# Performance work log

Measured on AMD Instinct MI355X. Metric: run time of the kernel, lower is better.

The kernel has to match this reference:

```python
import jax, jax.numpy as jnp
import numpy as np

NEG_INF = -1e9  # matches the TF additive-mask constant


def setup_inputs() -> dict:
    key = jax.random.key(0)
    k1, k2, k3 = jax.random.split(key, 3)
    B, Tq, Tk, D = 8, 2048, 2048, 1024
    decoder_outputs = jax.random.normal(k1, (B, Tq, D), dtype=jnp.float32)
    encoder_outputs = jax.random.normal(k2, (B, Tk, D), dtype=jnp.float32)
    encoder_mask = jax.random.randint(k3, (B, Tk), 0, 2, dtype=jnp.int32)
    return {
        "decoder_outputs": decoder_outputs,
        "encoder_outputs": encoder_outputs,
        "encoder_mask": encoder_mask,
    }


def reference(decoder_outputs, encoder_outputs, encoder_mask):
    # score[b, q, k] = <dec[b, q], enc[b, k]>  (no 1/sqrt(d) scaling in original)
    score = jnp.einsum("bqd,bkd->bqk", decoder_outputs, encoder_outputs)
    m = encoder_mask.astype(score.dtype)[:, None, :]  # [B, 1, Tk]
    score = score + (1.0 - m) * NEG_INF
    attention_weights = jax.nn.softmax(score, axis=-1)
    context_vector = jnp.einsum("bqk,bkd->bqd", attention_weights, encoder_outputs)
    return (context_vector, attention_weights)
```

## Files before the change

### kernel.cpp

```cpp
#include <hip/hip_runtime.h>
#include <cstddef>
#include <cstdint>

typedef _Float16 f16x8 __attribute__((ext_vector_type(8)));
typedef _Float16 f16x4 __attribute__((ext_vector_type(4)));
typedef float f32x4 __attribute__((ext_vector_type(4)));

static constexpr int BATCH = 8;
static constexpr int TQ = 2048;
static constexpr int TK = 2048;
static constexpr int DIM = 1024;
static constexpr size_t CTX_ELEMS = (size_t)BATCH * TQ * DIM;
static constexpr size_t ATT_ELEMS = (size_t)BATCH * TQ * TK;

static constexpr size_t WS_DEC = 0;
static constexpr size_t WS_ENC = WS_DEC + CTX_ELEMS;
static constexpr size_t WS_ENCT = WS_ENC + CTX_ELEMS;
static constexpr size_t WS_W = WS_ENCT + CTX_ELEMS;
static constexpr size_t WS_NEEDED_BYTES = (WS_W + ATT_ELEMS) * 2;

__device__ __forceinline__ void async16(const void* g, const void* l) {
  __builtin_amdgcn_global_load_lds(
      (const __attribute__((address_space(1))) unsigned int*)g,
      (__attribute__((address_space(3))) unsigned int*)l, 16, 0, 0);
}

__device__ __forceinline__ f16x8 cvt8(float4 a, float4 b) {
  f16x8 h;
  h[0] = (_Float16)a.x; h[1] = (_Float16)a.y; h[2] = (_Float16)a.z; h[3] = (_Float16)a.w;
  h[4] = (_Float16)b.x; h[5] = (_Float16)b.y; h[6] = (_Float16)b.z; h[7] = (_Float16)b.w;
  return h;
}


__global__ __launch_bounds__(256) void convert_dec_kernel(
    const float* __restrict__ dec, _Float16* __restrict__ dec16) {
  size_t i = ((size_t)blockIdx.x * 256 + threadIdx.x) * 8;
  float4 a = *(const float4*)(dec + i);
  float4 b = *(const float4*)(dec + i + 4);
  *(f16x8*)(dec16 + i) = cvt8(a, b);
}

__global__ __launch_bounds__(256) void convert_enc_kernel(
    const float* __restrict__ enc, _Float16* __restrict__ enc16,
    _Float16* __restrict__ encT) {
  __shared__ _Float16 sT[64 * 72];
  const int k0 = blockIdx.x * 64, d0 = blockIdx.y * 64, b = blockIdx.z;
  const int t = threadIdx.x;
  const int krow = t >> 2;
  const int dcol = (t & 3) * 16;

  const float* src = enc + ((size_t)b * TK + k0 + krow) * DIM + d0 + dcol;
  float4 f0 = *(const float4*)(src);
  float4 f1 = *(const float4*)(src + 4);
  float4 f2 = *(const float4*)(src + 8);
  float4 f3 = *(const float4*)(src + 12);
  _Float16 h[16];
#pragma unroll
  for (int i = 0; i < 4; i++) {
    h[i]      = (_Float16)((&f0.x)[i]);
    h[i + 4]  = (_Float16)((&f1.x)[i]);
    h[i + 8]  = (_Float16)((&f2.x)[i]);
    h[i + 12] = (_Float16)((&f3.x)[i]);
  }
  _Float16* dsts = enc16 + ((size_t)b * TK + k0 + krow) * DIM + d0 + dcol;
  *(f16x8*)dsts = *(const f16x8*)&h[0];
  *(f16x8*)(dsts + 8) = *(const f16x8*)&h[8];
#pragma unroll
  for (int i = 0; i < 16; i++)
    sT[(dcol + i) * 72 + krow] = h[i];
  __syncthreads();

  const int drow = t >> 2;
  const int kg = (t & 3) * 16;
  f16x8 v0 = *(const f16x8*)&sT[drow * 72 + kg];
  f16x8 v1 = *(const f16x8*)&sT[drow * 72 + kg + 8];
  _Float16* dst = encT + ((size_t)b * DIM + d0 + drow) * TK + k0 + kg;
  *(f16x8*)dst = v0;
  *(f16x8*)(dst + 8) = v1;
}

template <int M, int N, int K>
__global__ __launch_bounds__(256, 2) void gemm_nt(
    const _Float16* __restrict__ A, const _Float16* __restrict__ B,
    float* __restrict__ C) {
  __shared__ _Float16 sA[2][256 * 32];
  __shared__ _Float16 sB[2][128 * 32];

  const int b = blockIdx.x, nt = blockIdx.y, mt = blockIdx.z;
  const int t = threadIdx.x;
  const int lane = t & 63, w = t >> 6;
  const int tm = lane & 15, quad = lane >> 4;

  const _Float16* Ab = A + ((size_t)b * M + mt * 256) * K;
  const _Float16* Bb = B + ((size_t)b * N + nt * 128) * K;

  const int srow = lane >> 2;
  const int scol = (lane & 3) * 8;

  f32x4 acc[4][8] = {};

  for (int k0 = 0; k0 < K; k0 += 64) {
    __syncthreads();
#pragma unroll
    for (int s = 0; s < 2; s++) {
#pragma unroll
      for (int i = 0; i < 4; i++)
        async16(Ab + (size_t)(w * 64 + 16 * i + srow) * K + k0 + s * 32 + scol,
                &sA[s][(w * 64 + 16 * i) * 32]);
#pragma unroll
      for (int i = 0; i < 2; i++)
        async16(Bb + (size_t)(w * 32 + 16 * i + srow) * K + k0 + s * 32 + scol,
                &sB[s][(w * 32 + 16 * i) * 32]);
    }
    __syncthreads();

#pragma unroll
    for (int s = 0; s < 2; s++) {
      f16x8 aF[4], bF[8];
#pragma unroll
      for (int i = 0; i < 4; i++)
        aF[i] = *(const f16x8*)&sA[s][(w * 64 + i * 16 + tm) * 32 + quad * 8];
#pragma unroll
      for (int j = 0; j < 8; j++)
        bF[j] = *(const f16x8*)&sB[s][(j * 16 + tm) * 32 + quad * 8];

#pragma unroll
      for (int i = 0; i < 4; i++)
#pragma unroll
        for (int j = 0; j < 8; j++)
          acc[i][j] = __builtin_amdgcn_mfma_f32_16x16x32_f16(aF[i], bF[j], acc[i][j], 0, 0, 0);
    }
  }

#pragma unroll
  for (int i = 0; i < 4; i++) {
#pragma unroll
    for (int rr = 0; rr < 4; rr++) {
      size_t rowoff = ((size_t)b * M + mt * 256 + w * 64 + i * 16 + quad * 4 + rr) * (size_t)N;
#pragma unroll
      for (int j = 0; j < 8; j++)
        C[rowoff + nt * 128 + j * 16 + tm] = acc[i][j][rr];
    }
  }
}

__global__ __launch_bounds__(256) void softmax_kernel(
    float* __restrict__ S, const int* __restrict__ mask, _Float16* __restrict__ W16) {
  const int row = blockIdx.x;
  const int b = row >> 11;
  float* srow = S + (size_t)row * TK;
  const int* mrow = mask + (size_t)b * TK;
  const int t = threadIdx.x;

  float4 s0 = *(const float4*)(srow + t * 8);
  float4 s1 = *(const float4*)(srow + t * 8 + 4);
  int4 m0 = *(const int4*)(mrow + t * 8);
  int4 m1 = *(const int4*)(mrow + t * 8 + 4);

  float v[8] = {s0.x, s0.y, s0.z, s0.w, s1.x, s1.y, s1.z, s1.w};
  const int mm[8] = {m0.x, m0.y, m0.z, m0.w, m1.x, m1.y, m1.z, m1.w};
#pragma unroll
  for (int i = 0; i < 8; i++)
    if (!mm[i]) v[i] += -1e9f;

  float mx = v[0];
#pragma unroll
  for (int i = 1; i < 8; i++) mx = fmaxf(mx, v[i]);
#pragma unroll
  for (int off = 32; off > 0; off >>= 1) mx = fmaxf(mx, __shfl_down(mx, off));

  __shared__ float redm[4];
  __shared__ float reds[4];
  if ((t & 63) == 0) redm[t >> 6] = mx;
  __syncthreads();
  mx = fmaxf(fmaxf(redm[0], redm[1]), fmaxf(redm[2], redm[3]));

  float e[8];
  float lsum = 0.f;
#pragma unroll
  for (int i = 0; i < 8; i++) {
    e[i] = __expf(v[i] - mx);
    lsum += e[i];
  }
#pragma unroll
  for (int off = 32; off > 0; off >>= 1) lsum += __shfl_down(lsum, off);
  if ((t & 63) == 0) reds[t >> 6] = lsum;
  __syncthreads();
  const float inv = 1.0f / (reds[0] + reds[1] + reds[2] + reds[3]);

  float4 o0 = {e[0] * inv, e[1] * inv, e[2] * inv, e[3] * inv};
  float4 o1 = {e[4] * inv, e[5] * inv, e[6] * inv, e[7] * inv};
  *(float4*)(srow + t * 8) = o0;
  *(float4*)(srow + t * 8 + 4) = o1;
  if (W16) {
    f16x8 h;
    h[0] = (_Float16)o0.x; h[1] = (_Float16)o0.y; h[2] = (_Float16)o0.z; h[3] = (_Float16)o0.w;
    h[4] = (_Float16)o1.x; h[5] = (_Float16)o1.y; h[6] = (_Float16)o1.z; h[7] = (_Float16)o1.w;
    *(f16x8*)(W16 + (size_t)row * TK + t * 8) = h;
  }
}

static constexpr int BM = 128, BN = 128, BK = 32;
static constexpr int LDSS = 40;

__global__ __launch_bounds__(256) void score_kernel_fb(
    const float* __restrict__ dec, const float* __restrict__ enc,
    float* __restrict__ S) {
  __shared__ _Float16 sA[BM * LDSS];
  __shared__ _Float16 sB[BN * LDSS];
  const int nt = blockIdx.x, mt = blockIdx.y, b = blockIdx.z;
  const int t = threadIdx.x;
  const int lane = t & 63, wave = t >> 6;
  const int wm = wave >> 1, wn = wave & 1;
  const int tm = lane & 15, quad = lane >> 4;
  const float* Abase = dec + ((size_t)b * TQ + mt * BM) * DIM;
  const float* Bbase = enc + ((size_t)b * TK + nt * BN) * DIM;
  f32x4 acc[4][4] = {};
  const int r = t >> 2;
  const int c8 = (t & 3) * 8;
  for (int k0 = 0; k0 < DIM; k0 += BK) {
    float4 a0 = *(const float4*)(Abase + (size_t)r * DIM + k0 + c8);
    float4 a1 = *(const float4*)(Abase + (size_t)r * DIM + k0 + c8 + 4);
    float4 a2 = *(const float4*)(Abase + (size_t)(r + 64) * DIM + k0 + c8);
    float4 a3 = *(const float4*)(Abase + (size_t)(r + 64) * DIM + k0 + c8 + 4);
    float4 b0 = *(const float4*)(Bbase + (size_t)r * DIM + k0 + c8);
    float4 b1 = *(const float4*)(Bbase + (size_t)r * DIM + k0 + c8 + 4);
    float4 b2 = *(const float4*)(Bbase + (size_t)(r + 64) * DIM + k0 + c8);
    float4 b3 = *(const float4*)(Bbase + (size_t)(r + 64) * DIM + k0 + c8 + 4);
    __syncthreads();
    *(f16x8*)&sA[r * LDSS + c8] = cvt8(a0, a1);
    *(f16x8*)&sA[(r + 64) * LDSS + c8] = cvt8(a2, a3);
    *(f16x8*)&sB[r * LDSS + c8] = cvt8(b0, b1);
    *(f16x8*)&sB[(r + 64) * LDSS + c8] = cvt8(b2, b3);
    __syncthreads();
    f16x8 aF[4], bF[4];
#pragma unroll
    for (int i = 0; i < 4; i++)
      aF[i] = *(const f16x8*)&sA[(wm * 64 + i * 16 + tm) * LDSS + quad * 8];
#pragma unroll
    for (int j = 0; j < 4; j++)
      bF[j] = *(const f16x8*)&sB[(wn * 64 + j * 16 + tm) * LDSS + quad * 8];
#pragma unroll
    for (int i = 0; i < 4; i++)
#pragma unroll
      for (int j = 0; j < 4; j++)
        acc[i][j] = __builtin_amdgcn_mfma_f32_16x16x32_f16(aF[i], bF[j], acc[i][j], 0, 0, 0);
  }
#pragma unroll
  for (int i = 0; i < 4; i++) {
#pragma unroll
    for (int rr = 0; rr < 4; rr++) {
      size_t rowoff = ((size_t)b * TQ + mt * BM + wm * 64 + i * 16 + quad * 4 + rr) * (size_t)TK;
#pragma unroll
      for (int j = 0; j < 4; j++)
        S[rowoff + nt * BN + wn * 64 + j * 16 + tm] = acc[i][j][rr];
    }
  }
}

__global__ __launch_bounds__(256) void ctx_kernel_fb(
    const float* __restrict__ W, const float* __restrict__ enc,
    float* __restrict__ C) {
  __shared__ _Float16 sA[BM * LDSS];
  __shared__ _Float16 sB[BN * LDSS];
  const int nt = blockIdx.x;
  const int mt = blockIdx.y;
  const int b = blockIdx.z;
  const int t = threadIdx.x;
  const int lane = t & 63, wave = t >> 6;
  const int wm = wave >> 1, wn = wave & 1;
  const int tm = lane & 15, quad = lane >> 4;
  const float* Abase = W + ((size_t)b * TQ + mt * BM) * TK;
  const float* Ebase = enc + (size_t)b * TK * DIM + nt * BN;
  f32x4 acc[4][4] = {};
  const int r = t >> 2;
  const int c8 = (t & 3) * 8;
  const int kkB = (t & 7) * 4;
  const int nnB = (t >> 3) * 4;
  for (int k0 = 0; k0 < TK; k0 += BK) {
    float4 a0 = *(const float4*)(Abase + (size_t)r * TK + k0 + c8);
    float4 a1 = *(const float4*)(Abase + (size_t)r * TK + k0 + c8 + 4);
    float4 a2 = *(const float4*)(Abase + (size_t)(r + 64) * TK + k0 + c8);
    float4 a3 = *(const float4*)(Abase + (size_t)(r + 64) * TK + k0 + c8 + 4);
    float4 f[4];
#pragma unroll
    for (int i = 0; i < 4; i++)
      f[i] = *(const float4*)(Ebase + (size_t)(k0 + kkB + i) * DIM + nnB);
    __syncthreads();
    *(f16x8*)&sA[r * LDSS + c8] = cvt8(a0, a1);
    *(f16x8*)&sA[(r + 64) * LDSS + c8] = cvt8(a2, a3);
#pragma unroll
    for (int c = 0; c < 4; c++) {
      f16x4 h;
      h[0] = (_Float16)((&f[0].x)[c]);
      h[1] = (_Float16)((&f[1].x)[c]);
      h[2] = (_Float16)((&f[2].x)[c]);
      h[3] = (_Float16)((&f[3].x)[c]);
      *(f16x4*)&sB[(nnB + c) * LDSS + kkB] = h;
    }
    __syncthreads();
    f16x8 aF[4], bF[4];
#pragma unroll
    for (int i = 0; i < 4; i++)
      aF[i] = *(const f16x8*)&sA[(wm * 64 + i * 16 + tm) * LDSS + quad * 8];
#pragma unroll
    for (int j = 0; j < 4; j++)
      bF[j] = *(const f16x8*)&sB[(wn * 64 + j * 16 + tm) * LDSS + quad * 8];
#pragma unroll
    for (int i = 0; i < 4; i++)
#pragma unroll
      for (int j = 0; j < 4; j++)
        acc[i][j] = __builtin_amdgcn_mfma_f32_16x16x32_f16(aF[i], bF[j], acc[i][j], 0, 0, 0);
  }
#pragma unroll
  for (int i = 0; i < 4; i++) {
#pragma unroll
    for (int rr = 0; rr < 4; rr++) {
      size_t rowoff = ((size_t)b * TQ + mt * BM + wm * 64 + i * 16 + quad * 4 + rr) * (size_t)DIM;
#pragma unroll
      for (int j = 0; j < 4; j++)
        C[rowoff + nt * BN + wn * 64 + j * 16 + tm] = acc[i][j][rr];
    }
  }
}

extern "C" void kernel_launch(void* const* d_in, const int* in_sizes, int n_in,
                              void* d_out, int out_size, void* d_ws, size_t ws_size,
                              hipStream_t stream) {
  const float* dec = (const float*)d_in[0];
  const float* enc = (const float*)d_in[1];
  const int* mask = (const int*)d_in[2];

  float* ctx = (float*)d_out;
  float* attn = (float*)d_out + CTX_ELEMS;

  dim3 block(256);

  if (ws_size >= WS_NEEDED_BYTES) {
    _Float16* dec16 = (_Float16*)d_ws + WS_DEC;
    _Float16* enc16 = (_Float16*)d_ws + WS_ENC;
    _Float16* encT = (_Float16*)d_ws + WS_ENCT;
    _Float16* W16 = (_Float16*)d_ws + WS_W;

    convert_dec_kernel<<<dim3(CTX_ELEMS / (256 * 8)), block, 0, stream>>>(dec, dec16);
    convert_enc_kernel<<<dim3(TK / 64, DIM / 64, BATCH), block, 0, stream>>>(enc, enc16, encT);
    gemm_nt<TQ, TK, DIM><<<dim3(BATCH, TK / 128, TQ / 256), block, 0, stream>>>(dec16, enc16, attn);
    softmax_kernel<<<dim3(BATCH * TQ), block, 0, stream>>>(attn, mask, W16);
    gemm_nt<TQ, DIM, TK><<<dim3(BATCH, DIM / 128, TQ / 256), block, 0, stream>>>(W16, encT, ctx);
  } else {
    score_kernel_fb<<<dim3(TK / BN, TQ / BM, BATCH), block, 0, stream>>>(dec, enc, attn);
    softmax_kernel<<<dim3(BATCH * TQ), block, 0, stream>>>(attn, mask, nullptr);
    ctx_kernel_fb<<<dim3(DIM / BN, TQ / BM, BATCH), block, 0, stream>>>(attn, enc, ctx);
  }
}
```

Measured before the change: 502.7 us.

## Replace GEMM with 8-wave 256x256 tile kernel using software-pipelined LDS staging

Replaces the 256-thread 256x128-tile GEMM with a 512-thread, 8-wave kernel that computes 256x256 output tiles. Global-to-LDS async loads are split into half-K stages and issued two iterations ahead, with explicit vmcnt waits and barriers so loads overlap the MFMA work. It also raises MFMA issue priority around the compute blocks. The larger tile cuts global traffic per FLOP, but the 128 KB of LDS and the heavier register use may limit occupancy, and the hand-tuned waitcnt sequencing is fragile.

Measured after the change: 514.0 us. 2.2% more time.

```diff
diff --git a/kernel.cpp b/kernel.cpp
--- a/kernel.cpp
+++ b/kernel.cpp
@@ -80,67 +80,120 @@
   *(f16x8*)(dst + 8) = v1;
 }
 
+
+template <int KD>
+__device__ __forceinline__ void stage_half(const _Float16* __restrict__ Xb,
+                                           _Float16* slot, int khalf,
+                                           int w, int lane) {
+  const int kgl = w & 3;
+  const int rg0 = (w >> 2) * 2;
+  const _Float16* g = Xb + (size_t)(rg0 * 64 + lane) * KD + khalf + kgl * 8;
+  _Float16* l = slot + kgl * 2048 + rg0 * 512;
+  async16(g, l);
+  async16(g + (size_t)64 * KD, l + 512);
+}
+
+__device__ __forceinline__ void load4(f16x8 (&dst)[4], const _Float16* base) {
+#pragma unroll
+  for (int i = 0; i < 4; ++i) dst[i] = *(const f16x8*)(base + i * 128);
+}
+
+__device__ __forceinline__ void mfma16(f32x4 (&acc)[8][4], const f16x8 (&aF)[4],
+                                       const f16x8 (&bF)[4], int mh) {
+  __builtin_amdgcn_s_setprio(1);
+#pragma unroll
+  for (int i = 0; i < 4; ++i)
+#pragma unroll
+    for (int j = 0; j < 4; ++j)
+      acc[mh * 4 + i][j] = __builtin_amdgcn_mfma_f32_16x16x32_f16(
+          aF[i], bF[j], acc[mh * 4 + i][j], 0, 0, 0);
+  __builtin_amdgcn_s_setprio(0);
+}
+
 template <int M, int N, int K>
-__global__ __launch_bounds__(256, 2) void gemm_nt(
+__global__ __launch_bounds__(512, 2) void gemm8p(
     const _Float16* __restrict__ A, const _Float16* __restrict__ B,
     float* __restrict__ C) {
-  __shared__ _Float16 sA[2][256 * 32];
-  __shared__ _Float16 sB[2][128 * 32];
+  __shared__ _Float16 lds[65536];
+  constexpr int T = K / 64;
 
   const int b = blockIdx.x, nt = blockIdx.y, mt = blockIdx.z;
-  const int t = threadIdx.x;
-  const int lane = t & 63, w = t >> 6;
+  const int tid = threadIdx.x;
+  const int lane = tid & 63, w = tid >> 6;
   const int tm = lane & 15, quad = lane >> 4;
+  const int wr = w >> 2, wc = w & 3;
 
   const _Float16* Ab = A + ((size_t)b * M + mt * 256) * K;
-  const _Float16* Bb = B + ((size_t)b * N + nt * 128) * K;
-
-  const int srow = lane >> 2;
-  const int scol = (lane & 3) * 8;
-
-  f32x4 acc[4][8] = {};
-
-  for (int k0 = 0; k0 < K; k0 += 64) {
-    __syncthreads();
-#pragma unroll
-    for (int s = 0; s < 2; s++) {
-#pragma unroll
-      for (int i = 0; i < 4; i++)
-        async16(Ab + (size_t)(w * 64 + 16 * i + srow) * K + k0 + s * 32 + scol,
-                &sA[s][(w * 64 + 16 * i) * 32]);
-#pragma unroll
-      for (int i = 0; i < 2; i++)
-        async16(Bb + (size_t)(w * 32 + 16 * i + srow) * K + k0 + s * 32 + scol,
-                &sB[s][(w * 32 + 16 * i) * 32]);
-    }
-    __syncthreads();
-
-#pragma unroll
-    for (int s = 0; s < 2; s++) {
-      f16x8 aF[4], bF[8];
-#pragma unroll
-      for (int i = 0; i < 4; i++)
-        aF[i] = *(const f16x8*)&sA[s][(w * 64 + i * 16 + tm) * 32 + quad * 8];
-#pragma unroll
-      for (int j = 0; j < 8; j++)
-        bF[j] = *(const f16x8*)&sB[s][(j * 16 + tm) * 32 + quad * 8];
-
-#pragma unroll
-      for (int i = 0; i < 4; i++)
-#pragma unroll
-        for (int j = 0; j < 8; j++)
-          acc[i][j] = __builtin_amdgcn_mfma_f32_16x16x32_f16(aF[i], bF[j], acc[i][j], 0, 0, 0);
-    }
-  }
-
-#pragma unroll
-  for (int i = 0; i < 4; i++) {
-#pragma unroll
-    for (int rr = 0; rr < 4; rr++) {
-      size_t rowoff = ((size_t)b * M + mt * 256 + w * 64 + i * 16 + quad * 4 + rr) * (size_t)N;
-#pragma unroll
-      for (int j = 0; j < 8; j++)
-        C[rowoff + nt * 128 + j * 16 + tm] = acc[i][j][rr];
+  const _Float16* Bb = B + ((size_t)b * N + nt * 256) * K;
+
+  const int aBase = quad * 2048 + (wr * 128 + tm) * 8;
+  const int bBase = quad * 2048 + (wc * 64 + tm) * 8;
+
+  f32x4 acc[8][4] = {};
+
+  stage_half<K>(Ab, lds, 0, w, lane);
+  stage_half<K>(Bb, lds + 32768, 0, w, lane);
+  stage_half<K>(Ab, lds + 16384, 32, w, lane);
+  stage_half<K>(Bb, lds + 49152, 32, w, lane);
+  stage_half<K>(Ab, lds + 8192, 64, w, lane);
+  stage_half<K>(Bb, lds + 32768 + 8192, 64, w, lane);
+  asm volatile("s_waitcnt vmcnt(8)" ::: "memory");
+  __builtin_amdgcn_s_barrier();
+
+  for (int t = 0; t < T; ++t) {
+    const int p = t & 1, np = p ^ 1;
+    _Float16* const aLo = lds + p * 8192;
+    _Float16* const aHi = lds + 16384 + p * 8192;
+    _Float16* const bLo = lds + 32768 + p * 8192;
+    _Float16* const bHi = lds + 49152 + p * 8192;
+    const bool s1 = (t + 1 < T), s2 = (t + 2 < T);
+    f16x8 aF[4], bF[4];
+
+    load4(aF, aLo + aBase);
+    load4(bF, bLo + bBase);
+    if (s1) stage_half<K>(Ab, lds + 16384 + np * 8192, (t + 1) * 64 + 32, w, lane);
+    __builtin_amdgcn_s_barrier();
+    mfma16(acc, aF, bF, 0);
+    __builtin_amdgcn_s_barrier();
+
+    load4(aF, aLo + aBase + 512);
+    if (s1) {
+      stage_half<K>(Bb, lds + 49152 + np * 8192, (t + 1) * 64 + 32, w, lane);
+      asm volatile("s_waitcnt vmcnt(8)" ::: "memory");
+    } else {
+      asm volatile("s_waitcnt vmcnt(0)" ::: "memory");
+    }
+    __builtin_amdgcn_s_barrier();
+    mfma16(acc, aF, bF, 1);
+    __builtin_amdgcn_s_barrier();
+
+    load4(aF, aHi + aBase);
+    load4(bF, bHi + bBase);
+    if (s2) stage_half<K>(Ab, lds + p * 8192, (t + 2) * 64, w, lane);
+    __builtin_amdgcn_s_barrier();
+    mfma16(acc, aF, bF, 0);
+    __builtin_amdgcn_s_barrier();
+
+    load4(aF, aHi + aBase + 512);
+    if (s2) {
+      stage_half<K>(Bb, lds + 32768 + p * 8192, (t + 2) * 64, w, lane);
+      asm volatile("s_waitcnt vmcnt(8)" ::: "memory");
+    } else if (t + 2 == T) {
+      asm volatile("s_waitcnt vmcnt(4)" ::: "memory");
+    }
+    __builtin_amdgcn_s_barrier();
+    mfma16(acc, aF, bF, 1);
+    __builtin_amdgcn_s_barrier();
+  }
+
+#pragma unroll
+  for (int i = 0; i < 8; ++i) {
+#pragma unroll
+    for (int rr = 0; rr < 4; ++rr) {
+      size_t row = (size_t)b * M + mt * 256 + wr * 128 + i * 16 + quad * 4 + rr;
+      float* Crow = C + row * (size_t)N + nt * 256 + wc * 64 + tm;
+#pragma unroll
+      for (int j = 0; j < 4; ++j) Crow[j * 16] = acc[i][j][rr];
     }
   }
 }
@@ -345,9 +398,9 @@
 
     convert_dec_kernel<<<dim3(CTX_ELEMS / (256 * 8)), block, 0, stream>>>(dec, dec16);
     convert_enc_kernel<<<dim3(TK / 64, DIM / 64, BATCH), block, 0, stream>>>(enc, enc16, encT);
-    gemm_nt<TQ, TK, DIM><<<dim3(BATCH, TK / 128, TQ / 256), block, 0, stream>>>(dec16, enc16, attn);
+    gemm8p<TQ, TK, DIM><<<dim3(BATCH, TK / 256, TQ / 256), dim3(512), 0, stream>>>(dec16, enc16, attn);
     softmax_kernel<<<dim3(BATCH * TQ), block, 0, stream>>>(attn, mask, W16);
-    gemm_nt<TQ, DIM, TK><<<dim3(BATCH, DIM / 128, TQ / 256), block, 0, stream>>>(W16, encT, ctx);
+    gemm8p<TQ, DIM, TK><<<dim3(BATCH, DIM / 256, TQ / 256), dim3(512), 0, stream>>>(W16, encT, ctx);
   } else {
     score_kernel_fb<<<dim3(TK / BN, TQ / BM, BATCH), block, 0, stream>>>(dec, enc, attn);
     softmax_kernel<<<dim3(BATCH * TQ), block, 0, stream>>>(attn, mask, nullptr);
```

## Fuse decoder fp32-to-fp16 conversion into the score GEMM A-tile load

Applied to the files above, without the earlier changes.

Removes the standalone decoder conversion kernel and its fp16 workspace. The score GEMM now reads fp32 decoder rows into registers, converts them to fp16 and stores them into LDS, prefetching the next K step in registers while MFMAs run. This saves a full write and re-read of the fp16 decoder copy. In exchange the GEMM reads twice the A bytes per tile (re-read across the 16 N tiles) and holds 64 extra VGPRs for prefetch, which may hurt occupancy or cache behaviour.

Result: slower. 519.5 us (+3.3%).

```diff
diff --git a/kernel.cpp b/kernel.cpp
--- a/kernel.cpp
+++ b/kernel.cpp
@@ -13,8 +13,7 @@
 static constexpr size_t CTX_ELEMS = (size_t)BATCH * TQ * DIM;
 static constexpr size_t ATT_ELEMS = (size_t)BATCH * TQ * TK;
 
-static constexpr size_t WS_DEC = 0;
-static constexpr size_t WS_ENC = WS_DEC + CTX_ELEMS;
+static constexpr size_t WS_ENC = 0;
 static constexpr size_t WS_ENCT = WS_ENC + CTX_ELEMS;
 static constexpr size_t WS_W = WS_ENCT + CTX_ELEMS;
 static constexpr size_t WS_NEEDED_BYTES = (WS_W + ATT_ELEMS) * 2;
@@ -32,14 +31,6 @@
   return h;
 }
 
-
-__global__ __launch_bounds__(256) void convert_dec_kernel(
-    const float* __restrict__ dec, _Float16* __restrict__ dec16) {
-  size_t i = ((size_t)blockIdx.x * 256 + threadIdx.x) * 8;
-  float4 a = *(const float4*)(dec + i);
-  float4 b = *(const float4*)(dec + i + 4);
-  *(f16x8*)(dec16 + i) = cvt8(a, b);
-}
 
 __global__ __launch_bounds__(256) void convert_enc_kernel(
     const float* __restrict__ enc, _Float16* __restrict__ enc16,
@@ -78,6 +69,96 @@
   _Float16* dst = encT + ((size_t)b * DIM + d0 + drow) * TK + k0 + kg;
   *(f16x8*)dst = v0;
   *(f16x8*)(dst + 8) = v1;
+}
+
+__global__ __launch_bounds__(256, 2) void gemm1_kernel(
+    const float* __restrict__ dec, const _Float16* __restrict__ B,
+    float* __restrict__ C) {
+  constexpr int M = TQ, N = TK, K = DIM;
+  __shared__ _Float16 sA[2][256 * 32];
+  __shared__ _Float16 sB[2][128 * 32];
+
+  const int b = blockIdx.x, nt = blockIdx.y, mt = blockIdx.z;
+  const int t = threadIdx.x;
+  const int lane = t & 63, w = t >> 6;
+  const int tm = lane & 15, quad = lane >> 4;
+
+  const float* Ab = dec + ((size_t)b * M + mt * 256) * K;
+  const _Float16* Bb = B + ((size_t)b * N + nt * 128) * K;
+
+  const int srow = lane >> 2;
+  const int scol = (lane & 3) * 8;
+
+  const int arow = t >> 3;
+  const int acol = (t & 7) * 4;
+
+  f32x4 acc[4][8] = {};
+  float4 areg[16];
+
+#pragma unroll
+  for (int s = 0; s < 2; s++)
+#pragma unroll
+    for (int bt = 0; bt < 8; bt++)
+      areg[s * 8 + bt] =
+          *(const float4*)(Ab + (size_t)(bt * 32 + arow) * K + s * 32 + acol);
+
+  for (int k0 = 0; k0 < K; k0 += 64) {
+    __syncthreads();
+#pragma unroll
+    for (int s = 0; s < 2; s++)
+#pragma unroll
+      for (int i = 0; i < 2; i++)
+        async16(Bb + (size_t)(w * 32 + 16 * i + srow) * K + k0 + s * 32 + scol,
+                &sB[s][(w * 32 + 16 * i) * 32]);
+#pragma unroll
+    for (int s = 0; s < 2; s++)
+#pragma unroll
+      for (int bt = 0; bt < 8; bt++) {
+        float4 a = areg[s * 8 + bt];
+        f16x4 h;
+        h[0] = (_Float16)a.x; h[1] = (_Float16)a.y;
+        h[2] = (_Float16)a.z; h[3] = (_Float16)a.w;
+        *(f16x4*)&sA[s][(bt * 32 + arow) * 32 + acol] = h;
+      }
+    __syncthreads();
+
+    if (k0 + 64 < K) {
+#pragma unroll
+      for (int s = 0; s < 2; s++)
+#pragma unroll
+        for (int bt = 0; bt < 8; bt++)
+          areg[s * 8 + bt] = *(const float4*)(
+              Ab + (size_t)(bt * 32 + arow) * K + (k0 + 64) + s * 32 + acol);
+    }
+
+#pragma unroll
+    for (int s = 0; s < 2; s++) {
+      f16x8 aF[4], bF[8];
+#pragma unroll
+      for (int i = 0; i < 4; i++)
+        aF[i] = *(const f16x8*)&sA[s][(w * 64 + i * 16 + tm) * 32 + quad * 8];
+#pragma unroll
+      for (int j = 0; j < 8; j++)
+        bF[j] = *(const f16x8*)&sB[s][(j * 16 + tm) * 32 + quad * 8];
+
+#pragma unroll
+      for (int i = 0; i < 4; i++)
+#pragma unroll
+        for (int j = 0; j < 8; j++)
+          acc[i][j] = __builtin_amdgcn_mfma_f32_16x16x32_f16(aF[i], bF[j], acc[i][j], 0, 0, 0);
+    }
+  }
+
+#pragma unroll
+  for (int i = 0; i < 4; i++) {
+#pragma unroll
+    for (int rr = 0; rr < 4; rr++) {
+      size_t rowoff = ((size_t)b * M + mt * 256 + w * 64 + i * 16 + quad * 4 + rr) * (size_t)N;
+#pragma unroll
+      for (int j = 0; j < 8; j++)
+        C[rowoff + nt * 128 + j * 16 + tm] = acc[i][j][rr];
+    }
+  }
 }
 
 template <int M, int N, int K>
@@ -338,14 +419,12 @@
   dim3 block(256);
 
   if (ws_size >= WS_NEEDED_BYTES) {
-    _Float16* dec16 = (_Float16*)d_ws + WS_DEC;
     _Float16* enc16 = (_Float16*)d_ws + WS_ENC;
     _Float16* encT = (_Float16*)d_ws + WS_ENCT;
     _Float16* W16 = (_Float16*)d_ws + WS_W;
 
-    convert_dec_kernel<<<dim3(CTX_ELEMS / (256 * 8)), block, 0, stream>>>(dec, dec16);
     convert_enc_kernel<<<dim3(TK / 64, DIM / 64, BATCH), block, 0, stream>>>(enc, enc16, encT);
-    gemm_nt<TQ, TK, DIM><<<dim3(BATCH, TK / 128, TQ / 256), block, 0, stream>>>(dec16, enc16, attn);
+    gemm1_kernel<<<dim3(BATCH, TK / 128, TQ / 256), block, 0, stream>>>(dec, enc16, attn);
     softmax_kernel<<<dim3(BATCH * TQ), block, 0, stream>>>(attn, mask, W16);
     gemm_nt<TQ, DIM, TK><<<dim3(BATCH, DIM / 128, TQ / 256), block, 0, stream>>>(W16, encT, ctx);
   } else {
```

## Shrink GEMM tile to 128x128 with 2x2 warps, swizzle LDS, fuse converts

Applied to the files above, without the earlier changes.

The GEMM kernel moves from a 256x128 tile, where each warp owns 64 rows, to a 128x128 tile split 2x2 across warps. This lowers register use and allows 4 blocks per CU, giving more blocks for occupancy. Shared-memory staging now uses an XOR swizzle on the 16-byte chunk index to reduce LDS bank conflicts on fragment reads. The dec and enc conversion kernels are merged into one launch, which saves a kernel launch. The smaller tile means less reuse per block and more global traffic for the same work.

After: 512.4 us. Within noise of the previous version (+1.9%).

```diff
diff --git a/kernel.cpp b/kernel.cpp
--- a/kernel.cpp
+++ b/kernel.cpp
@@ -33,17 +33,10 @@
 }
 
 
-__global__ __launch_bounds__(256) void convert_dec_kernel(
-    const float* __restrict__ dec, _Float16* __restrict__ dec16) {
-  size_t i = ((size_t)blockIdx.x * 256 + threadIdx.x) * 8;
-  float4 a = *(const float4*)(dec + i);
-  float4 b = *(const float4*)(dec + i + 4);
-  *(f16x8*)(dec16 + i) = cvt8(a, b);
-}
-
-__global__ __launch_bounds__(256) void convert_enc_kernel(
-    const float* __restrict__ enc, _Float16* __restrict__ enc16,
-    _Float16* __restrict__ encT) {
+__global__ __launch_bounds__(256) void convert_kernel(
+    const float* __restrict__ enc, const float* __restrict__ dec,
+    _Float16* __restrict__ enc16, _Float16* __restrict__ encT,
+    _Float16* __restrict__ dec16) {
   __shared__ _Float16 sT[64 * 72];
   const int k0 = blockIdx.x * 64, d0 = blockIdx.y * 64, b = blockIdx.z;
   const int t = threadIdx.x;
@@ -69,6 +62,18 @@
 #pragma unroll
   for (int i = 0; i < 16; i++)
     sT[(dcol + i) * 72 + krow] = h[i];
+
+  {
+    const int bid = ((blockIdx.z * gridDim.y) + blockIdx.y) * gridDim.x + blockIdx.x;
+    size_t base = (size_t)bid * 4096 + (size_t)t * 16;
+    float4 a0 = *(const float4*)(dec + base);
+    float4 a1 = *(const float4*)(dec + base + 4);
+    float4 a2 = *(const float4*)(dec + base + 8);
+    float4 a3 = *(const float4*)(dec + base + 12);
+    *(f16x8*)(dec16 + base) = cvt8(a0, a1);
+    *(f16x8*)(dec16 + base + 8) = cvt8(a2, a3);
+  }
+
   __syncthreads();
 
   const int drow = t >> 2;
@@ -81,55 +86,60 @@
 }
 
 template <int M, int N, int K>
-__global__ __launch_bounds__(256, 2) void gemm_nt(
+__global__ __launch_bounds__(256, 4) void gemm97(
     const _Float16* __restrict__ A, const _Float16* __restrict__ B,
     float* __restrict__ C) {
-  __shared__ _Float16 sA[2][256 * 32];
+  __shared__ _Float16 sA[2][128 * 32];
   __shared__ _Float16 sB[2][128 * 32];
 
   const int b = blockIdx.x, nt = blockIdx.y, mt = blockIdx.z;
   const int t = threadIdx.x;
   const int lane = t & 63, w = t >> 6;
   const int tm = lane & 15, quad = lane >> 4;
-
-  const _Float16* Ab = A + ((size_t)b * M + mt * 256) * K;
+  const int wm = w >> 1, wn = w & 1;
+
+  const _Float16* Ab = A + ((size_t)b * M + mt * 128) * K;
   const _Float16* Bb = B + ((size_t)b * N + nt * 128) * K;
 
   const int srow = lane >> 2;
-  const int scol = (lane & 3) * 8;
-
-  f32x4 acc[4][8] = {};
+  const int schunk = (lane & 3) ^ (srow & 3);
+
+  const int xorc = (quad ^ (tm & 3)) * 8;
+  const int aBase = (wm * 64 + tm) * 32 + xorc;
+  const int bBase = (wn * 64 + tm) * 32 + xorc;
+
+  f32x4 acc[4][4] = {};
 
   for (int k0 = 0; k0 < K; k0 += 64) {
     __syncthreads();
 #pragma unroll
     for (int s = 0; s < 2; s++) {
 #pragma unroll
+      for (int j = 0; j < 2; j++) {
+        const int row0 = 16 * (j * 4 + w);
+        async16(Ab + (size_t)(row0 + srow) * K + k0 + s * 32 + schunk * 8,
+                &sA[s][row0 * 32]);
+        async16(Bb + (size_t)(row0 + srow) * K + k0 + s * 32 + schunk * 8,
+                &sB[s][row0 * 32]);
+      }
+    }
+    __syncthreads();
+
+#pragma unroll
+    for (int s = 0; s < 2; s++) {
+      f16x8 aF[4], bF[4];
+#pragma unroll
       for (int i = 0; i < 4; i++)
-        async16(Ab + (size_t)(w * 64 + 16 * i + srow) * K + k0 + s * 32 + scol,
-                &sA[s][(w * 64 + 16 * i) * 32]);
-#pragma unroll
-      for (int i = 0; i < 2; i++)
-        async16(Bb + (size_t)(w * 32 + 16 * i + srow) * K + k0 + s * 32 + scol,
-                &sB[s][(w * 32 + 16 * i) * 32]);
-    }
-    __syncthreads();
-
-#pragma unroll
-    for (int s = 0; s < 2; s++) {
-      f16x8 aF[4], bF[8];
+        aF[i] = *(const f16x8*)&sA[s][aBase + i * 512];
+#pragma unroll
+      for (int j = 0; j < 4; j++)
+        bF[j] = *(const f16x8*)&sB[s][bBase + j * 512];
 #pragma unroll
       for (int i = 0; i < 4; i++)
-        aF[i] = *(const f16x8*)&sA[s][(w * 64 + i * 16 + tm) * 32 + quad * 8];
-#pragma unroll
-      for (int j = 0; j < 8; j++)
-        bF[j] = *(const f16x8*)&sB[s][(j * 16 + tm) * 32 + quad * 8];
-
-#pragma unroll
-      for (int i = 0; i < 4; i++)
-#pragma unroll
-        for (int j = 0; j < 8; j++)
-          acc[i][j] = __builtin_amdgcn_mfma_f32_16x16x32_f16(aF[i], bF[j], acc[i][j], 0, 0, 0);
+#pragma unroll
+        for (int j = 0; j < 4; j++)
+          acc[i][j] = __builtin_amdgcn_mfma_f32_16x16x32_f16(
+              aF[i], bF[j], acc[i][j], 0, 0, 0);
     }
   }
 
@@ -137,10 +147,10 @@
   for (int i = 0; i < 4; i++) {
 #pragma unroll
     for (int rr = 0; rr < 4; rr++) {
-      size_t rowoff = ((size_t)b * M + mt * 256 + w * 64 + i * 16 + quad * 4 + rr) * (size_t)N;
-#pragma unroll
-      for (int j = 0; j < 8; j++)
-        C[rowoff + nt * 128 + j * 16 + tm] = acc[i][j][rr];
+      size_t row = (size_t)b * M + mt * 128 + wm * 64 + i * 16 + quad * 4 + rr;
+      float* Crow = C + row * (size_t)N + nt * 128 + wn * 64 + tm;
+#pragma unroll
+      for (int j = 0; j < 4; j++) Crow[j * 16] = acc[i][j][rr];
     }
   }
 }
@@ -343,11 +353,11 @@
     _Float16* encT = (_Float16*)d_ws + WS_ENCT;
     _Float16* W16 = (_Float16*)d_ws + WS_W;
 
-    convert_dec_kernel<<<dim3(CTX_ELEMS / (256 * 8)), block, 0, stream>>>(dec, dec16);
-    convert_enc_kernel<<<dim3(TK / 64, DIM / 64, BATCH), block, 0, stream>>>(enc, enc16, encT);
-    gemm_nt<TQ, TK, DIM><<<dim3(BATCH, TK / 128, TQ / 256), block, 0, stream>>>(dec16, enc16, attn);
+    convert_kernel<<<dim3(TK / 64, DIM / 64, BATCH), block, 0, stream>>>(
+        enc, dec, enc16, encT, dec16);
+    gemm97<TQ, TK, DIM><<<dim3(BATCH, TK / 128, TQ / 128), block, 0, stream>>>(dec16, enc16, attn);
     softmax_kernel<<<dim3(BATCH * TQ), block, 0, stream>>>(attn, mask, W16);
-    gemm_nt<TQ, DIM, TK><<<dim3(BATCH, DIM / 128, TQ / 256), block, 0, stream>>>(W16, encT, ctx);
+    gemm97<TQ, DIM, TK><<<dim3(BATCH, DIM / 128, TQ / 128), block, 0, stream>>>(W16, encT, ctx);
   } else {
     score_kernel_fb<<<dim3(TK / BN, TQ / BM, BATCH), block, 0, stream>>>(dec, enc, attn);
     softmax_kernel<<<dim3(BATCH * TQ), block, 0, stream>>>(attn, mask, nullptr);
```
